# Kernel optimization log

Hardware: AMD Instinct MI355X
Metric: run time of the kernel (lower is better)

The kernel has to match this reference:

```python
import jax, jax.numpy as jnp
import numpy as np

B, CIN, COUT, K, S, P, D = 4, 128, 128, 3, 1, 1, 1
H = W = 96
MASK_SCALE = 2.0


def setup_inputs() -> dict:
    key = jax.random.key(0)
    k1, k2, k3, k4 = jax.random.split(key, 4)
    x = jax.random.normal(k1, (B, CIN, H, W), jnp.float32)
    weight = jax.random.normal(k2, (COUT, CIN, K, K), jnp.float32) * 0.05
    bias = jax.random.normal(k3, (COUT,), jnp.float32) * 0.05
    # conv_offset_mask: out_channels = deformable_groups*3*K*K = 27, no bias
    w_offmask = jax.random.normal(k4, (3 * K * K, CIN, K, K), jnp.float32) * 0.01
    return {"x": x, "weight": weight, "bias": bias, "w_offmask": w_offmask}


def _bilinear_gather(x, py, px):
    """x: [B,C,H,W]; py,px: [B,K2,Ho,Wo] float sample coords.
    Returns [B,C,K2,Ho,Wo], zero outside image (per-corner validity as in DCNv2)."""
    Bn, C, Hh, Ww = x.shape
    K2, Ho, Wo = py.shape[1], py.shape[2], py.shape[3]
    y0 = jnp.floor(py); x0 = jnp.floor(px)
    ly = py - y0; lx = px - x0
    y0i = y0.astype(jnp.int32); x0i = x0.astype(jnp.int32)
    y1i = y0i + 1; x1i = x0i + 1
    x_flat = x.reshape(Bn, C, Hh * Ww)

    def corner(yi, xi, w):
        valid = (yi >= 0) & (yi < Hh) & (xi >= 0) & (xi < Ww)
        yc = jnp.clip(yi, 0, Hh - 1)
        xc = jnp.clip(xi, 0, Ww - 1)
        idx = (yc * Ww + xc).reshape(Bn, K2 * Ho * Wo)
        v = jnp.take_along_axis(x_flat, idx[:, None, :], axis=2)  # [B,C,K2*Ho*Wo]
        v = v.reshape(Bn, C, K2, Ho, Wo)
        wv = (w * valid.astype(x.dtype))[:, None]  # [B,1,K2,Ho,Wo]
        return v * wv

    out = corner(y0i, x0i, (1 - ly) * (1 - lx))
    out = out + corner(y0i, x1i, (1 - ly) * lx)
    out = out + corner(y1i, x0i, ly * (1 - lx))
    out = out + corner(y1i, x1i, ly * lx)
    return out


def reference(x, weight, bias, w_offmask):
    K2 = K * K
    # offset/mask conv (standard conv, no bias)
    om = jax.lax.conv_general_dilated(
        x, w_offmask, window_strides=(S, S), padding=[(P, P), (P, P)],
        dimension_numbers=("NCHW", "OIHW", "NCHW"))  # [B, 3*K2, Ho, Wo]
    o1 = om[:, :K2]
    o2 = om[:, K2:2 * K2]
    mask = jax.nn.sigmoid(om[:, 2 * K2:]) * MASK_SCALE  # [B,K2,Ho,Wo]
    offset = jnp.concatenate([o1, o2], axis=1)  # [B,2*K2,Ho,Wo]

    Ho, Wo = om.shape[2], om.shape[3]
    ki, kj = jnp.meshgrid(jnp.arange(K), jnp.arange(K), indexing="ij")
    ki = ki.reshape(K2); kj = kj.reshape(K2)
    ho = jnp.arange(Ho); wo = jnp.arange(Wo)
    base_y = (ho[None, :] * S - P + ki[:, None] * D).astype(x.dtype)  # [K2,Ho]
    base_x = (wo[None, :] * S - P + kj[:, None] * D).astype(x.dtype)  # [K2,Wo]
    py = base_y[None, :, :, None] + o1  # [B,K2,Ho,Wo]
    px = base_x[None, :, None, :] + o2

    sampled = _bilinear_gather(x, py, px)            # [B,C,K2,Ho,Wo]
    sampled = sampled * mask[:, None]                # modulation
    wr = weight.reshape(COUT, CIN, K2)
    out = jnp.einsum("ock,bckhw->bohw", wr, sampled) + bias[None, :, None, None]
    return out, offset
```

## Files before the change

### kernel.cpp

```cpp
#include <hip/hip_runtime.h>
#include <math.h>

#define HH 96
#define WW 96
#define HW (96*96)
#define CIN_ 128
#define COUT_ 128
#define OUT_ELEMS (4*128*96*96)
#define TPX 48

#define XT_OFF   0u
#define WBF_OFF  9437184u
#define WOMB_OFF 9732096u

typedef __attribute__((ext_vector_type(8))) short short8v;
typedef __attribute__((ext_vector_type(4))) float float4v;

__device__ __forceinline__ unsigned short f2bf(float f) {
    unsigned u = __builtin_bit_cast(unsigned, f);
    u += 0x7FFFu + ((u >> 16) & 1u);
    return (unsigned short)(u >> 16);
}
__device__ __forceinline__ float bflo(unsigned u) {
    return __builtin_bit_cast(float, u << 16);
}
__device__ __forceinline__ float bfhi(unsigned u) {
    return __builtin_bit_cast(float, u & 0xffff0000u);
}

__global__ __launch_bounds__(256) void pre_kernel(
    const float* __restrict__ x, const float* __restrict__ w,
    const float* __restrict__ wom, unsigned short* __restrict__ xt,
    unsigned short* __restrict__ wbf, unsigned short* __restrict__ womb)
{
    __shared__ float tile[64][130];
    const int t = threadIdx.x;

    if (blockIdx.x < 576) {
        const int b  = blockIdx.x / 144;
        const int p0 = (blockIdx.x - b * 144) * 64;
#pragma unroll
        for (int j = 0; j < 8; j++) {
            const int i  = j * 256 + t;
            const int c  = i >> 4;
            const int p4 = (i & 15) * 4;
            const float4 v = *(const float4*)(x + ((size_t)(b * CIN_ + c) * HW + p0 + p4));
            tile[p4 + 0][c] = v.x; tile[p4 + 1][c] = v.y;
            tile[p4 + 2][c] = v.z; tile[p4 + 3][c] = v.w;
        }
        __syncthreads();
#pragma unroll
        for (int j = 0; j < 8; j++) {
            const int i   = j * 256 + t;
            const int pxl = i >> 5;
            const int c4  = (i & 31) * 4;
            uint2 v;
            v.x = (unsigned)f2bf(tile[pxl][c4 + 0]) | ((unsigned)f2bf(tile[pxl][c4 + 1]) << 16);
            v.y = (unsigned)f2bf(tile[pxl][c4 + 2]) | ((unsigned)f2bf(tile[pxl][c4 + 3]) << 16);
            *(uint2*)(xt + ((size_t)(b * HW + p0 + pxl) * CIN_ + c4)) = v;
        }
    } else {
        const int i = (blockIdx.x - 576) * 256 + t;
        if (i < COUT_ * 1152) {
            const int oc = i / 1152, r = i - oc * 1152;
            const int kc = r >> 7, c = r & 127;
            wbf[i] = f2bf(w[(size_t)oc * 1152 + c * 9 + kc]);
        } else {
            const int i2 = i - COUT_ * 1152;
            if (i2 < 32 * 1152) {
                const int row = i2 / 1152, r = i2 - row * 1152;
                const int kc = r >> 7, c = r & 127;
                womb[i2] = (row < 27) ? f2bf(wom[(size_t)row * 1152 + c * 9 + kc]) : 0;
            }
        }
    }
}

__global__ __launch_bounds__(512, 6) void dconv_fused(
    const unsigned short* __restrict__ xt, const unsigned short* __restrict__ wbf,
    const unsigned short* __restrict__ womb, const float* __restrict__ bias,
    float* __restrict__ out, float* __restrict__ off_out)
{
    __shared__ int sprep[432 * 8];
    __shared__ int btile[2][TPX * 64];
    float* som = (float*)&btile[0][0];

    const int t    = threadIdx.x;
    const int wave = __builtin_amdgcn_readfirstlane(t >> 6);
    const int lane = t & 63;
    const int quad = lane >> 4;
    const int m    = lane & 15;
    const int b    = blockIdx.y;
    const int p0   = blockIdx.x * TPX;

    const unsigned short* xtb = xt + (size_t)b * HW * CIN_;

    if (wave < 6) {
        const int pxg = wave >> 1;
        const int mt  = wave & 1;
        const int pgl = pxg * 16 + m;
        const int pg  = p0 + pgl;
        const int h   = pg / 96;
        const int w   = pg - h * 96;

        float4v acc2;
#pragma unroll
        for (int r = 0; r < 4; r++) acc2[r] = 0.f;
        const short8v zerov = (short8v)0;

#pragma unroll
        for (int kc = 0; kc < 9; kc++) {
            const int ki = kc / 3, kj = kc - 3 * (kc / 3);
            const int y  = h + ki - 1, xx = w + kj - 1;
            const bool valid = ((unsigned)y < 96u) && ((unsigned)xx < 96u);
            const unsigned short* brow = xtb + (size_t)(y * 96 + xx) * CIN_ + quad * 8;
            const short* abase = (const short*)womb + (size_t)(mt * 16 + m) * 1152 + kc * 128 + quad * 8;
#pragma unroll
            for (int kst = 0; kst < 4; kst++) {
                const short8v bfv = valid ? *(const short8v*)(brow + kst * 32) : zerov;
                const short8v av  = *(const short8v*)(abase + kst * 32);
                acc2 = __builtin_amdgcn_mfma_f32_16x16x32_bf16(av, bfv, acc2, 0, 0, 0);
            }
        }
#pragma unroll
        for (int r = 0; r < 4; r++) {
            const int oc = mt * 16 + quad * 4 + r;
            if (oc < 27) som[oc * TPX + pgl] = acc2[r];
            if (oc < 18) off_out[(size_t)(b * 18 + oc) * HW + pg] = acc2[r];
        }
    }
    __syncthreads();

    if (t < 432) {
        const int kc  = t / 48;
        const int pxl = t - kc * 48;
        const int pg  = p0 + pxl;
        const int h   = pg / 96;
        const int w   = pg - h * 96;
        const int ki  = kc / 3, kj = kc - 3 * (kc / 3);

        const float o1 = som[kc * TPX + pxl];
        const float o2 = som[(9 + kc) * TPX + pxl];
        const float mr = som[(18 + kc) * TPX + pxl];
        const float mk = 2.f / (1.f + __expf(-mr));

        const float py = (float)(h - 1 + ki) + o1;
        const float px = (float)(w - 1 + kj) + o2;
        const float y0f = floorf(py), x0f = floorf(px);
        const float ly = py - y0f,    lx = px - x0f;
        const int y0 = (int)y0f, x0 = (int)x0f;
        const int y1 = y0 + 1,   x1 = x0 + 1;

        const float w00 = (1.f - ly) * (1.f - lx), w01 = (1.f - ly) * lx;
        const float w10 = ly * (1.f - lx),         w11 = ly * lx;

        const int yc0 = min(max(y0, 0), HH - 1), yc1 = min(max(y1, 0), HH - 1);
        const int xc0 = min(max(x0, 0), WW - 1), xc1 = min(max(x1, 0), WW - 1);
        const bool vy0 = (y0 >= 0) && (y0 < HH), vy1 = (y1 >= 0) && (y1 < HH);
        const bool vx0 = (x0 >= 0) && (x0 < WW), vx1 = (x1 >= 0) && (x1 < WW);

        sprep[t * 8 + 0] = yc0 * 96 + xc0;
        sprep[t * 8 + 1] = yc0 * 96 + xc1;
        sprep[t * 8 + 2] = yc1 * 96 + xc0;
        sprep[t * 8 + 3] = yc1 * 96 + xc1;
        sprep[t * 8 + 4] = __builtin_bit_cast(int, (vy0 && vx0) ? mk * w00 : 0.f);
        sprep[t * 8 + 5] = __builtin_bit_cast(int, (vy0 && vx1) ? mk * w01 : 0.f);
        sprep[t * 8 + 6] = __builtin_bit_cast(int, (vy1 && vx0) ? mk * w10 : 0.f);
        sprep[t * 8 + 7] = __builtin_bit_cast(int, (vy1 && vx1) ? mk * w11 : 0.f);
    }
    __syncthreads();

    float4v acc[3];
#pragma unroll
    for (int j = 0; j < 3; j++)
#pragma unroll
        for (int r = 0; r < 4; r++) acc[j][r] = 0.f;

    for (int kc = 0; kc < 9; kc++) {
        int* bt = &btile[kc & 1][0];

        const short* abase = (const short*)wbf + (size_t)(wave * 16 + m) * 1152 + kc * 128 + quad * 8;
        short8v af[4];
#pragma unroll
        for (int kst = 0; kst < 4; kst++)
            af[kst] = *(const short8v*)(abase + kst * 32);

#pragma unroll
        for (int p = 0; p < 6; p++) {
            const int pxl = p * 8 + wave;
            const int s   = kc * 48 + pxl;
            const int4   id4 = *(const int4*)&sprep[s * 8];
            const float4 w4  = *(const float4*)&sprep[s * 8 + 4];
            const unsigned u0 = *(const unsigned*)(xtb + (size_t)id4.x * CIN_ + 2 * lane);
            const unsigned u1 = *(const unsigned*)(xtb + (size_t)id4.y * CIN_ + 2 * lane);
            const unsigned u2 = *(const unsigned*)(xtb + (size_t)id4.z * CIN_ + 2 * lane);
            const unsigned u3 = *(const unsigned*)(xtb + (size_t)id4.w * CIN_ + 2 * lane);
            const float vx = w4.x * bflo(u0) + w4.y * bflo(u1) + w4.z * bflo(u2) + w4.w * bflo(u3);
            const float vy = w4.x * bfhi(u0) + w4.y * bfhi(u1) + w4.z * bfhi(u2) + w4.w * bfhi(u3);
            bt[pxl * 64 + (((lane >> 2) ^ (pxl & 7)) << 2) + (lane & 3)] =
                (int)((unsigned)f2bf(vx) | ((unsigned)f2bf(vy) << 16));
        }
        __syncthreads();

#pragma unroll
        for (int kst = 0; kst < 4; kst++) {
#pragma unroll
            for (int nt = 0; nt < 3; nt++) {
                const int pxl = nt * 16 + m;
                const short8v bfv = *(const short8v*)((const short*)bt
                    + 2 * (pxl * 64 + (((kst * 4 + quad) ^ (m & 7)) << 2)));
                acc[nt] = __builtin_amdgcn_mfma_f32_16x16x32_bf16(af[kst], bfv, acc[nt], 0, 0, 0);
            }
        }
    }

#pragma unroll
    for (int r = 0; r < 4; r++) {
        const int oc = wave * 16 + quad * 4 + r;
        const float bv = bias[oc];
#pragma unroll
        for (int nt = 0; nt < 3; nt++)
            out[(size_t)(b * COUT_ + oc) * HW + p0 + nt * 16 + m] = acc[nt][r] + bv;
    }
}

extern "C" void kernel_launch(void* const* d_in, const int* in_sizes, int n_in,
                              void* d_out, int out_size, void* d_ws, size_t ws_size,
                              hipStream_t stream) {
    const float* x      = (const float*)d_in[0];
    const float* weight = (const float*)d_in[1];
    const float* bias   = (const float*)d_in[2];
    const float* wom    = (const float*)d_in[3];

    float* out     = (float*)d_out;
    float* off_out = out + OUT_ELEMS;

    unsigned short* xtb  = (unsigned short*)((char*)d_ws + XT_OFF);
    unsigned short* wbf  = (unsigned short*)((char*)d_ws + WBF_OFF);
    unsigned short* womb = (unsigned short*)((char*)d_ws + WOMB_OFF);

    pre_kernel <<<dim3(1296),   256, 0, stream>>>(x, weight, wom, xtb, wbf, womb);
    dconv_fused<<<dim3(192, 4), 512, 0, stream>>>(xtb, wbf, womb, bias, out, off_out);
}
```

Measured before the change: 153.8 us.

## Software-pipeline bilinear gathers across kc steps and remap blocks across XCDs

The gather loop now issues its 8-byte-per-lane corner loads one step ahead into a register ring buffer, so the global latency of the next kc's gathers overlaps the current combine and MFMA work. Each lane now handles four channels and half-waves handle separate pixels. Both kernels remap their flat block index so neighbouring tiles land on the same XCD for better L2 locality. bf16 packing uses a perm instruction, and A-fragments are loaded per kst instead of all up front. The risk is higher register pressure from the ring buffer under the launch bound of 512 threads with 6 waves per SIMD, which could cause spills.

```diff
diff --git a/kernel.cpp b/kernel.cpp
--- a/kernel.cpp
+++ b/kernel.cpp
@@ -21,6 +21,13 @@
     u += 0x7FFFu + ((u >> 16) & 1u);
     return (unsigned short)(u >> 16);
 }
+__device__ __forceinline__ unsigned rneu(float f) {
+    unsigned u = __builtin_bit_cast(unsigned, f);
+    return u + 0x7FFFu + ((u >> 16) & 1u);
+}
+__device__ __forceinline__ unsigned pkbf(float hi, float lo) {
+    return __builtin_amdgcn_perm(rneu(hi), rneu(lo), 0x07060302u);
+}
 __device__ __forceinline__ float bflo(unsigned u) {
     return __builtin_bit_cast(float, u << 16);
 }
@@ -35,10 +42,12 @@
 {
     __shared__ float tile[64][130];
     const int t = threadIdx.x;
-
-    if (blockIdx.x < 576) {
-        const int b  = blockIdx.x / 144;
-        const int p0 = (blockIdx.x - b * 144) * 64;
+    const int f = blockIdx.x;
+
+    if (f < 576) {
+        const int g  = (f & 7) * 72 + (f >> 3);
+        const int b  = g / 144;
+        const int p0 = (g - b * 144) * 64;
 #pragma unroll
         for (int j = 0; j < 8; j++) {
             const int i  = j * 256 + t;
@@ -55,12 +64,12 @@
             const int pxl = i >> 5;
             const int c4  = (i & 31) * 4;
             uint2 v;
-            v.x = (unsigned)f2bf(tile[pxl][c4 + 0]) | ((unsigned)f2bf(tile[pxl][c4 + 1]) << 16);
-            v.y = (unsigned)f2bf(tile[pxl][c4 + 2]) | ((unsigned)f2bf(tile[pxl][c4 + 3]) << 16);
+            v.x = pkbf(tile[pxl][c4 + 1], tile[pxl][c4 + 0]);
+            v.y = pkbf(tile[pxl][c4 + 3], tile[pxl][c4 + 2]);
             *(uint2*)(xt + ((size_t)(b * HW + p0 + pxl) * CIN_ + c4)) = v;
         }
     } else {
-        const int i = (blockIdx.x - 576) * 256 + t;
+        const int i = (f - 576) * 256 + t;
         if (i < COUT_ * 1152) {
             const int oc = i / 1152, r = i - oc * 1152;
             const int kc = r >> 7, c = r & 127;
@@ -81,17 +90,24 @@
     const unsigned short* __restrict__ womb, const float* __restrict__ bias,
     float* __restrict__ out, float* __restrict__ off_out)
 {
-    __shared__ int sprep[432 * 8];
-    __shared__ int btile[2][TPX * 64];
-    float* som = (float*)&btile[0][0];
+    __shared__ int smem[9600];
+    int*   sprep  = smem;
+    int*   btile0 = smem + 3456;
+    int*   btile1 = smem + 6528;
+    float* som    = (float*)btile0;
 
     const int t    = threadIdx.x;
     const int wave = __builtin_amdgcn_readfirstlane(t >> 6);
     const int lane = t & 63;
     const int quad = lane >> 4;
     const int m    = lane & 15;
-    const int b    = blockIdx.y;
-    const int p0   = blockIdx.x * TPX;
+    const int l32  = lane & 31;
+    const int half = lane >> 5;
+
+    const int f  = blockIdx.x;
+    const int c  = (f & 7) * 96 + (f >> 3);
+    const int b  = c / 192;
+    const int p0 = (c - b * 192) * TPX;
 
     const unsigned short* xtb = xt + (size_t)b * HW * CIN_;
 
@@ -170,49 +186,68 @@
     }
     __syncthreads();
 
+    uint2 gbuf[3][4];
+
+#define ISSUE(SL, KCV, ITV) do {                                              \
+    const int pxl_ = wave * 6 + (ITV) * 2 + half;                             \
+    const int4 id4_ = *(const int4*)&sprep[((KCV) * 48 + pxl_) * 8];          \
+    const unsigned co_ = (unsigned)l32 << 3;                                  \
+    gbuf[SL][0] = *(const uint2*)((const char*)xtb + (((unsigned)id4_.x << 8) | co_)); \
+    gbuf[SL][1] = *(const uint2*)((const char*)xtb + (((unsigned)id4_.y << 8) | co_)); \
+    gbuf[SL][2] = *(const uint2*)((const char*)xtb + (((unsigned)id4_.z << 8) | co_)); \
+    gbuf[SL][3] = *(const uint2*)((const char*)xtb + (((unsigned)id4_.w << 8) | co_)); \
+} while (0)
+
+#define COMBINE(SL, IV) do {                                                  \
+    const int pxl_ = wave * 6 + (IV) * 2 + half;                              \
+    const float4 w4_ = *(const float4*)&sprep[(kc * 48 + pxl_) * 8 + 4];      \
+    const uint2 u0 = gbuf[SL][0], u1 = gbuf[SL][1];                           \
+    const uint2 u2 = gbuf[SL][2], u3 = gbuf[SL][3];                           \
+    const float v0 = w4_.x*bflo(u0.x) + w4_.y*bflo(u1.x) + w4_.z*bflo(u2.x) + w4_.w*bflo(u3.x); \
+    const float v1 = w4_.x*bfhi(u0.x) + w4_.y*bfhi(u1.x) + w4_.z*bfhi(u2.x) + w4_.w*bfhi(u3.x); \
+    const float v2 = w4_.x*bflo(u0.y) + w4_.y*bflo(u1.y) + w4_.z*bflo(u2.y) + w4_.w*bflo(u3.y); \
+    const float v3 = w4_.x*bfhi(u0.y) + w4_.y*bfhi(u1.y) + w4_.z*bfhi(u2.y) + w4_.w*bfhi(u3.y); \
+    uint2 o_;                                                                 \
+    o_.x = pkbf(v1, v0);                                                      \
+    o_.y = pkbf(v3, v2);                                                      \
+    *(uint2*)&bt[pxl_ * 64 + (((l32 >> 1) ^ (pxl_ & 7)) << 2) + ((l32 & 1) << 1)] = o_; \
+} while (0)
+
     float4v acc[3];
 #pragma unroll
     for (int j = 0; j < 3; j++)
 #pragma unroll
         for (int r = 0; r < 4; r++) acc[j][r] = 0.f;
 
+    ISSUE(0, 0, 0);
+    ISSUE(1, 0, 1);
+
     for (int kc = 0; kc < 9; kc++) {
-        int* bt = &btile[kc & 1][0];
+        int* bt = (kc & 1) ? btile1 : btile0;
+
+        ISSUE(2, kc, 2);
+        COMBINE(0, 0);
+        if (kc < 8) ISSUE(0, kc + 1, 0);
+        COMBINE(1, 1);
+        if (kc < 8) ISSUE(1, kc + 1, 1);
+        COMBINE(2, 2);
+        __syncthreads();
 
         const short* abase = (const short*)wbf + (size_t)(wave * 16 + m) * 1152 + kc * 128 + quad * 8;
-        short8v af[4];
-#pragma unroll
-        for (int kst = 0; kst < 4; kst++)
-            af[kst] = *(const short8v*)(abase + kst * 32);
-
-#pragma unroll
-        for (int p = 0; p < 6; p++) {
-            const int pxl = p * 8 + wave;
-            const int s   = kc * 48 + pxl;
-            const int4   id4 = *(const int4*)&sprep[s * 8];
-            const float4 w4  = *(const float4*)&sprep[s * 8 + 4];
-            const unsigned u0 = *(const unsigned*)(xtb + (size_t)id4.x * CIN_ + 2 * lane);
-            const unsigned u1 = *(const unsigned*)(xtb + (size_t)id4.y * CIN_ + 2 * lane);
-            const unsigned u2 = *(const unsigned*)(xtb + (size_t)id4.z * CIN_ + 2 * lane);
-            const unsigned u3 = *(const unsigned*)(xtb + (size_t)id4.w * CIN_ + 2 * lane);
-            const float vx = w4.x * bflo(u0) + w4.y * bflo(u1) + w4.z * bflo(u2) + w4.w * bflo(u3);
-            const float vy = w4.x * bfhi(u0) + w4.y * bfhi(u1) + w4.z * bfhi(u2) + w4.w * bfhi(u3);
-            bt[pxl * 64 + (((lane >> 2) ^ (pxl & 7)) << 2) + (lane & 3)] =
-                (int)((unsigned)f2bf(vx) | ((unsigned)f2bf(vy) << 16));
-        }
-        __syncthreads();
-
 #pragma unroll
         for (int kst = 0; kst < 4; kst++) {
+            const short8v af = *(const short8v*)(abase + kst * 32);
 #pragma unroll
             for (int nt = 0; nt < 3; nt++) {
                 const int pxl = nt * 16 + m;
                 const short8v bfv = *(const short8v*)((const short*)bt
                     + 2 * (pxl * 64 + (((kst * 4 + quad) ^ (m & 7)) << 2)));
-                acc[nt] = __builtin_amdgcn_mfma_f32_16x16x32_bf16(af[kst], bfv, acc[nt], 0, 0, 0);
+                acc[nt] = __builtin_amdgcn_mfma_f32_16x16x32_bf16(af, bfv, acc[nt], 0, 0, 0);
             }
         }
     }
+#undef ISSUE
+#undef COMBINE
 
 #pragma unroll
     for (int r = 0; r < 4; r++) {
@@ -239,6 +274,6 @@
     unsigned short* wbf  = (unsigned short*)((char*)d_ws + WBF_OFF);
     unsigned short* womb = (unsigned short*)((char*)d_ws + WOMB_OFF);
 
-    pre_kernel <<<dim3(1296),   256, 0, stream>>>(x, weight, wom, xtb, wbf, womb);
-    dconv_fused<<<dim3(192, 4), 512, 0, stream>>>(xtb, wbf, womb, bias, out, off_out);
-}
+    pre_kernel <<<dim3(1296), 256, 0, stream>>>(x, weight, wom, xtb, wbf, womb);
+    dconv_fused<<<dim3(768),  512, 0, stream>>>(xtb, wbf, womb, bias, out, off_out);
+}
```

Result: slower. 159.0 us (+3.4%).
